# Optimization experiments

Hardware: AMD Instinct MI355X
Metric: run time of the kernel (lower is better)

Reference implementation:

```python
import jax, jax.numpy as jnp
import numpy as np

B, L, H, R, T = 2, 128, 768, 4, 3


def setup_inputs() -> dict:
    key = jax.random.key(0)
    ks = jax.random.split(key, 10)
    s = lambda k, shape: jax.random.normal(k, shape, dtype=jnp.float32) * 0.02
    return {
        "hidden_state": jax.random.normal(ks[0], (B, L, H), dtype=jnp.float32),
        "W_src": s(ks[1], (R * H, H)),
        "b_src": s(ks[2], (R * H,)),
        "W_tgt": s(ks[3], (R * H, H)),
        "b_tgt": s(ks[4], (R * H,)),
        "w_out": s(ks[5], (H,)),
        "dense_W": s(ks[6], (T * H, H)),
        "dense_b": s(ks[7], (T * H,)),
        "clf_W": s(ks[8], (1, H)),
        "clf_b": s(ks[9], (1,)),
    }


def reference(hidden_state, W_src, b_src, W_tgt, b_tgt, w_out,
              dense_W, dense_b, clf_W, clf_b):
    b, l, h = hidden_state.shape
    # Biaffine pairwise relation scoring (dropout = identity at eval).
    h_src = (hidden_state @ W_src.T + b_src).reshape(b, l, R, h)  # [B,L,R,H]
    h_tgt = (hidden_state @ W_tgt.T + b_tgt).reshape(b, l, R, h)  # [B,L,R,H]
    # Pairwise broadcast-add -> tanh -> reduce with w_out. [B,L,L,R,H] intermediate.
    pair = jnp.tanh(h_src[:, :, None, :, :] + h_tgt[:, None, :, :, :])
    relation_logits = jnp.einsum('bstrh,h->bstr', pair, w_out)
    relation_logits = jnp.transpose(relation_logits, (0, 3, 1, 2))  # [B,R,L,L]
    # Token binary classification head.
    z = (hidden_state @ dense_W.T + dense_b).reshape(b, l, T, h)   # [B,L,T,H]
    source_mask_logits = jnp.tanh(z) @ clf_W[0] + clf_b[0]          # [B,L,T]
    source_mask_logits = jnp.transpose(source_mask_logits, (0, 2, 1))  # [B,T,L]
    return relation_logits, source_mask_logits, h_src, h_tgt
```

## Files before the change

### kernel.cpp

```cpp
#include <hip/hip_runtime.h>
#include <hip/hip_bf16.h>

#define LL 128
#define HH 768
#define OFF_REL  0
#define OFF_MASK 131072
#define OFF_HSRC 131840
#define OFF_HTGT 918272
#define SCALEC 2.8853900817779268f

typedef __attribute__((ext_vector_type(8))) short short8;
typedef __attribute__((ext_vector_type(4))) float floatx4;

__device__ inline unsigned short f2bf(float f) {
  unsigned u = __float_as_uint(f);
  u += 0x7FFFu + ((u >> 16) & 1u);
  return (unsigned short)(u >> 16);
}
struct us4 { unsigned short x, y, z, w; };

__device__ __forceinline__ void gload16(const void* g, void* l) {
  __builtin_amdgcn_global_load_lds(
      (const __attribute__((address_space(1))) unsigned int*)g,
      (__attribute__((address_space(3))) unsigned int*)l,
      16, 0, 0);
}

__global__ __launch_bounds__(256) void cvt_kernel(
    const float4* __restrict__ hs, const float4* __restrict__ wsrc,
    const float4* __restrict__ wtgt, const float4* __restrict__ wd,
    us4* __restrict__ ab, us4* __restrict__ wb)
{
  const int n0 = 49152;
  const int n1 = n0 + 589824;
  const int n2 = n1 + 589824;
  const int n3 = n2 + 442368;
  int stride = gridDim.x * blockDim.x;
  for (int i = blockIdx.x * blockDim.x + threadIdx.x; i < n3; i += stride) {
    const float4* src; us4* dst;
    if (i < n0)      { src = hs   + i;        dst = ab + i; }
    else if (i < n1) { src = wsrc + (i - n0); dst = wb + (i - n0); }
    else if (i < n2) { src = wtgt + (i - n1); dst = wb + 589824 + (i - n1); }
    else             { src = wd   + (i - n2); dst = wb + 1179648 + (i - n2); }
    float4 v = *src;
    us4 o; o.x = f2bf(v.x); o.y = f2bf(v.y); o.z = f2bf(v.z); o.w = f2bf(v.w);
    *dst = o;
  }
}

__global__ __launch_bounds__(256, 2) void gemm_kernel(
    const unsigned short* __restrict__ Ab, const unsigned short* __restrict__ Wb,
    const float* __restrict__ b_src, const float* __restrict__ b_tgt,
    const float* __restrict__ dense_b,
    float* __restrict__ out, float* __restrict__ z,
    float* __restrict__ Es, float* __restrict__ Et)
{
  __shared__ __align__(1024) char sAB[4][16384];
  int tid = threadIdx.x;
  int wave = tid >> 6, lane = tid & 63;
  int nb = blockIdx.x, rb = blockIdx.y;
  int gcol0 = nb * 64, grow0 = rb * 64;
  int which = (nb < 48) ? 0 : (nb < 96) ? 1 : 2;

  int r0 = tid >> 3, c0 = tid & 7;
  int c0s = c0 ^ (r0 & 7);
  const unsigned short* gA0 = Ab + (long)(grow0 + r0) * HH + c0s * 8;
  const unsigned short* gA1 = gA0 + 32 * HH;
  const unsigned short* gB0 = Wb + (long)(gcol0 + r0) * HH + c0s * 8;
  const unsigned short* gB1 = gB0 + 32 * HH;

  int lr = lane & 15, hi = lane >> 4;
  int wm = (wave >> 1) * 32, wn = (wave & 1) * 32;
  int swz = lr & 7;

  floatx4 acc[2][2];
  #pragma unroll
  for (int mi = 0; mi < 2; ++mi)
    #pragma unroll
    for (int ni = 0; ni < 2; ++ni)
      acc[mi][ni] = (floatx4){0.f, 0.f, 0.f, 0.f};

#define STAGE(BUF, KT) do {                                       \
    char* b_ = &sAB[BUF][0];                                      \
    gload16(gA0 + (KT) * 64, b_ + wave * 1024);                   \
    gload16(gA1 + (KT) * 64, b_ + 4096 + wave * 1024);            \
    gload16(gB0 + (KT) * 64, b_ + 8192 + wave * 1024);            \
    gload16(gB1 + (KT) * 64, b_ + 12288 + wave * 1024);           \
  } while (0)

  STAGE(0, 0);
  STAGE(1, 1);
  STAGE(2, 2);

  #pragma unroll
  for (int kt = 0; kt < 12; ++kt) {
    int buf = kt & 3;
    if (kt <= 8) {
      STAGE((kt + 3) & 3, kt + 3);
      asm volatile("s_waitcnt vmcnt(12)" ::: "memory");
    } else if (kt == 9) {
      asm volatile("s_waitcnt vmcnt(8)" ::: "memory");
    } else if (kt == 10) {
      asm volatile("s_waitcnt vmcnt(4)" ::: "memory");
    } else {
      asm volatile("s_waitcnt vmcnt(0)" ::: "memory");
    }
    __builtin_amdgcn_sched_barrier(0);
    __builtin_amdgcn_s_barrier();
    __builtin_amdgcn_sched_barrier(0);

    const char* bA = &sAB[buf][0];
    const char* bB = bA + 8192;
    #pragma unroll
    for (int ks = 0; ks < 2; ++ks) {
      int cs = ((ks * 4 + hi) ^ swz) * 16;
      short8 a0 = *(const short8*)(bA + (wm + lr) * 128 + cs);
      short8 a1 = *(const short8*)(bA + (wm + 16 + lr) * 128 + cs);
      short8 b0 = *(const short8*)(bB + (wn + lr) * 128 + cs);
      short8 b1 = *(const short8*)(bB + (wn + 16 + lr) * 128 + cs);
      acc[0][0] = __builtin_amdgcn_mfma_f32_16x16x32_bf16(a0, b0, acc[0][0], 0, 0, 0);
      acc[0][1] = __builtin_amdgcn_mfma_f32_16x16x32_bf16(a0, b1, acc[0][1], 0, 0, 0);
      acc[1][0] = __builtin_amdgcn_mfma_f32_16x16x32_bf16(a1, b0, acc[1][0], 0, 0, 0);
      acc[1][1] = __builtin_amdgcn_mfma_f32_16x16x32_bf16(a1, b1, acc[1][1], 0, 0, 0);
    }

    __builtin_amdgcn_sched_barrier(0);
    __builtin_amdgcn_s_barrier();
  }
#undef STAGE

  int lrow = hi * 4;
  #pragma unroll
  for (int mi = 0; mi < 2; ++mi)
  #pragma unroll
  for (int ni = 0; ni < 2; ++ni) {
    int colg = gcol0 + wn + ni * 16 + lr;
    int row0 = grow0 + wm + mi * 16 + lrow;
    if (which == 0) {
      float bv = b_src[colg];
      #pragma unroll
      for (int r2 = 0; r2 < 4; ++r2) {
        int row = row0 + r2;
        float v = acc[mi][ni][r2] + bv;
        out[OFF_HSRC + row * 3072 + colg] = v;
        Es[row * 3072 + colg] = __builtin_amdgcn_exp2f(SCALEC * v);
      }
    } else if (which == 1) {
      int cc = colg - 3072;
      float bv = b_tgt[cc];
      #pragma unroll
      for (int r2 = 0; r2 < 4; ++r2) {
        int row = row0 + r2;
        float v = acc[mi][ni][r2] + bv;
        out[OFF_HTGT + row * 3072 + cc] = v;
        Et[row * 3072 + cc] = __builtin_amdgcn_exp2f(SCALEC * v);
      }
    } else {
      int cc = colg - 6144;
      float bv = dense_b[cc];
      #pragma unroll
      for (int r2 = 0; r2 < 4; ++r2)
        z[(row0 + r2) * 2304 + cc] = acc[mi][ni][r2] + bv;
    }
  }
}

#define PHC 256
__global__ __launch_bounds__(512) void pair_kernel(
    const float* __restrict__ Es, const float* __restrict__ Et,
    const float* __restrict__ w_out,
    const float* __restrict__ z, const float* __restrict__ clf_W,
    const float* __restrict__ clf_b, float* __restrict__ out)
{
  int tid = threadIdx.x;

  if (blockIdx.z == 8) {
    int blk = blockIdx.y * 8 + blockIdx.x;
    int wave = tid >> 6, lane = tid & 63;
    int slot = blk * 8 + wave;
    for (int o = slot; o < 768; o += 512) {
      int b = o / 384, rem = o - b * 384;
      int t = rem >> 7, lt = rem & 127;
      const float* zr = z + (long)(b * LL + lt) * 2304 + t * HH;
      float acc = 0.f;
      for (int h = lane; h < HH; h += 64) {
        float x = zr[h];
        float th = 1.f - 2.f * __builtin_amdgcn_rcpf(1.f + __builtin_amdgcn_exp2f(SCALEC * x));
        acc = fmaf(clf_W[h], th, acc);
      }
      #pragma unroll
      for (int d = 32; d; d >>= 1) acc += __shfl_down(acc, d);
      if (lane == 0) out[OFF_MASK + o] = acc + clf_b[0];
    }
    return;
  }

  __shared__ float sA[16][PHC + 4];
  __shared__ float sB[16][PHC + 4];
  __shared__ float sRed[2048];
  __shared__ float sWsum;

  int g = tid >> 6, lane = tid & 63;
  int sq = lane >> 3, tq = lane & 7;
  int t0 = blockIdx.x * 16, s0 = blockIdx.y * 16;
  int br = blockIdx.z, bb = br >> 2, r = br & 3;

  if (tid < 64) {
    float wsm = 0.f;
    for (int h = tid; h < HH; h += 64) wsm += w_out[h];
    #pragma unroll
    for (int d = 32; d; d >>= 1) wsm += __shfl_down(wsm, d);
    if (tid == 0) sWsum = wsm;
  }

  float a00 = 0.f, a01 = 0.f, a10 = 0.f, a11 = 0.f;

  for (int c = 0; c < HH; c += PHC) {
    int offu = __builtin_amdgcn_readfirstlane(c + g * 32);
    float4 wv[8];
    #pragma unroll
    for (int q = 0; q < 8; ++q) wv[q] = *(const float4*)(w_out + offu + q * 4);

    __syncthreads();
    #pragma unroll
    for (int j = 0; j < 2; ++j) {
      int idx = tid * 2 + j;
      int row = idx >> 6, col4 = (idx & 63) * 4;
      *(float4*)&sA[row][col4] =
          *(const float4*)(Es + (long)(bb * LL + s0 + row) * 3072 + r * HH + c + col4);
      *(float4*)&sB[row][col4] =
          *(const float4*)(Et + (long)(bb * LL + t0 + row) * 3072 + r * HH + c + col4);
    }
    __syncthreads();

    const float* pA0 = &sA[2 * sq][g * 32];
    const float* pA1 = &sA[2 * sq + 1][g * 32];
    const float* pB0 = &sB[2 * tq][g * 32];
    const float* pB1 = &sB[2 * tq + 1][g * 32];
    #pragma unroll
    for (int hh = 0; hh < 32; hh += 4) {
      float4 e0 = *(const float4*)(pA0 + hh);
      float4 e1 = *(const float4*)(pA1 + hh);
      float4 f0 = *(const float4*)(pB0 + hh);
      float4 f1 = *(const float4*)(pB1 + hh);
      float4 vw = wv[hh >> 2];
      a00 = fmaf(vw.x, __builtin_amdgcn_rcpf(fmaf(e0.x, f0.x, 1.f)), a00);
      a01 = fmaf(vw.x, __builtin_amdgcn_rcpf(fmaf(e0.x, f1.x, 1.f)), a01);
      a10 = fmaf(vw.x, __builtin_amdgcn_rcpf(fmaf(e1.x, f0.x, 1.f)), a10);
      a11 = fmaf(vw.x, __builtin_amdgcn_rcpf(fmaf(e1.x, f1.x, 1.f)), a11);
      a00 = fmaf(vw.y, __builtin_amdgcn_rcpf(fmaf(e0.y, f0.y, 1.f)), a00);
      a01 = fmaf(vw.y, __builtin_amdgcn_rcpf(fmaf(e0.y, f1.y, 1.f)), a01);
      a10 = fmaf(vw.y, __builtin_amdgcn_rcpf(fmaf(e1.y, f0.y, 1.f)), a10);
      a11 = fmaf(vw.y, __builtin_amdgcn_rcpf(fmaf(e1.y, f1.y, 1.f)), a11);
      a00 = fmaf(vw.z, __builtin_amdgcn_rcpf(fmaf(e0.z, f0.z, 1.f)), a00);
      a01 = fmaf(vw.z, __builtin_amdgcn_rcpf(fmaf(e0.z, f1.z, 1.f)), a01);
      a10 = fmaf(vw.z, __builtin_amdgcn_rcpf(fmaf(e1.z, f0.z, 1.f)), a10);
      a11 = fmaf(vw.z, __builtin_amdgcn_rcpf(fmaf(e1.z, f1.z, 1.f)), a11);
      a00 = fmaf(vw.w, __builtin_amdgcn_rcpf(fmaf(e0.w, f0.w, 1.f)), a00);
      a01 = fmaf(vw.w, __builtin_amdgcn_rcpf(fmaf(e0.w, f1.w, 1.f)), a01);
      a10 = fmaf(vw.w, __builtin_amdgcn_rcpf(fmaf(e1.w, f0.w, 1.f)), a10);
      a11 = fmaf(vw.w, __builtin_amdgcn_rcpf(fmaf(e1.w, f1.w, 1.f)), a11);
    }
  }

  sRed[0 * 512 + g * 64 + lane] = a00;
  sRed[1 * 512 + g * 64 + lane] = a01;
  sRed[2 * 512 + g * 64 + lane] = a10;
  sRed[3 * 512 + g * 64 + lane] = a11;
  __syncthreads();
  if (tid < 256) {
    int s = tid >> 4, t = tid & 15;
    int pp = (s >> 1) * 8 + (t >> 1);
    int sl = (s & 1) * 2 + (t & 1);
    float sum = 0.f;
    #pragma unroll
    for (int gg = 0; gg < 8; ++gg) sum += sRed[sl * 512 + gg * 64 + pp];
    out[((long)br * LL + (s0 + s)) * LL + (t0 + t)] = sWsum - 2.f * sum;
  }
}

extern "C" void kernel_launch(void* const* d_in, const int* in_sizes, int n_in,
                              void* d_out, int out_size, void* d_ws, size_t ws_size,
                              hipStream_t stream)
{
  const float* hidden  = (const float*)d_in[0];
  const float* W_src   = (const float*)d_in[1];
  const float* b_src   = (const float*)d_in[2];
  const float* W_tgt   = (const float*)d_in[3];
  const float* b_tgt   = (const float*)d_in[4];
  const float* w_out   = (const float*)d_in[5];
  const float* dense_W = (const float*)d_in[6];
  const float* dense_b = (const float*)d_in[7];
  const float* clf_W   = (const float*)d_in[8];
  const float* clf_b   = (const float*)d_in[9];
  float* out = (float*)d_out;
  char* ws = (char*)d_ws;

  unsigned short* Ab = (unsigned short*)ws;
  unsigned short* Wb = (unsigned short*)(ws + 393216);
  float* z  = (float*)(ws + 13369344);
  float* Es = (float*)(ws + 15728640);
  float* Et = (float*)(ws + 18874368);

  hipLaunchKernelGGL(cvt_kernel, dim3(2048), dim3(256), 0, stream,
      (const float4*)hidden, (const float4*)W_src, (const float4*)W_tgt,
      (const float4*)dense_W, (us4*)Ab, (us4*)Wb);
  hipLaunchKernelGGL(gemm_kernel, dim3(132, 4), dim3(256), 0, stream,
      Ab, Wb, b_src, b_tgt, dense_b, out, z, Es, Et);
  hipLaunchKernelGGL(pair_kernel, dim3(8, 8, 9), dim3(512), 0, stream,
      Es, Et, w_out, z, clf_W, clf_b, out + OFF_REL);
}
```

Measured before the change: 43.80 us.

## Store exp intermediates in bf16 and stage full hidden rows in LDS once

The GEMM epilogue now writes the exponentiated source and target projections as bf16 rather than fp32, halving that intermediate's write and read traffic. The pair kernel loads all 768 hidden columns for its 16x16 tile into shared memory in one pass, removing the three-chunk loop and its per-chunk barriers. w_out is also staged in LDS. The cost is lower precision in the exp values feeding the tanh reconstruction, a larger LDS footprint, and extra unpack work from bf16 to fp32 in the inner loop.

```diff
diff --git a/kernel.cpp b/kernel.cpp
--- a/kernel.cpp
+++ b/kernel.cpp
@@ -16,6 +16,9 @@
   unsigned u = __float_as_uint(f);
   u += 0x7FFFu + ((u >> 16) & 1u);
   return (unsigned short)(u >> 16);
+}
+__device__ __forceinline__ float bf2f(unsigned short u) {
+  return __uint_as_float(((unsigned)u) << 16);
 }
 struct us4 { unsigned short x, y, z, w; };
 
@@ -53,7 +56,7 @@
     const float* __restrict__ b_src, const float* __restrict__ b_tgt,
     const float* __restrict__ dense_b,
     float* __restrict__ out, float* __restrict__ z,
-    float* __restrict__ Es, float* __restrict__ Et)
+    unsigned short* __restrict__ Esb, unsigned short* __restrict__ Etb)
 {
   __shared__ __align__(1024) char sAB[4][16384];
   int tid = threadIdx.x;
@@ -143,7 +146,7 @@
         int row = row0 + r2;
         float v = acc[mi][ni][r2] + bv;
         out[OFF_HSRC + row * 3072 + colg] = v;
-        Es[row * 3072 + colg] = __builtin_amdgcn_exp2f(SCALEC * v);
+        Esb[row * 3072 + colg] = f2bf(__builtin_amdgcn_exp2f(SCALEC * v));
       }
     } else if (which == 1) {
       int cc = colg - 3072;
@@ -153,7 +156,7 @@
         int row = row0 + r2;
         float v = acc[mi][ni][r2] + bv;
         out[OFF_HTGT + row * 3072 + cc] = v;
-        Et[row * 3072 + cc] = __builtin_amdgcn_exp2f(SCALEC * v);
+        Etb[row * 3072 + cc] = f2bf(__builtin_amdgcn_exp2f(SCALEC * v));
       }
     } else {
       int cc = colg - 6144;
@@ -165,9 +168,9 @@
   }
 }
 
-#define PHC 256
+#define PADW 776
 __global__ __launch_bounds__(512) void pair_kernel(
-    const float* __restrict__ Es, const float* __restrict__ Et,
+    const unsigned short* __restrict__ Esb, const unsigned short* __restrict__ Etb,
     const float* __restrict__ w_out,
     const float* __restrict__ z, const float* __restrict__ clf_W,
     const float* __restrict__ clf_b, float* __restrict__ out)
@@ -195,8 +198,9 @@
     return;
   }
 
-  __shared__ float sA[16][PHC + 4];
-  __shared__ float sB[16][PHC + 4];
+  __shared__ unsigned short sA[16][PADW];
+  __shared__ unsigned short sB[16][PADW];
+  __shared__ __align__(16) float sW[768];
   __shared__ float sRed[2048];
   __shared__ float sWsum;
 
@@ -212,54 +216,46 @@
     for (int d = 32; d; d >>= 1) wsm += __shfl_down(wsm, d);
     if (tid == 0) sWsum = wsm;
   }
+  if (tid >= 64 && tid < 256) *(float4*)&sW[(tid - 64) * 4] = *(const float4*)(w_out + (tid - 64) * 4);
+
+  #pragma unroll
+  for (int j = 0; j < 3; ++j) {
+    int idx = j * 512 + tid;
+    int row = idx / 96, c8 = idx - row * 96;
+    *(uint4*)&sA[row][c8 * 8] =
+        *(const uint4*)(Esb + (long)(bb * LL + s0 + row) * 3072 + r * HH + c8 * 8);
+    *(uint4*)&sB[row][c8 * 8] =
+        *(const uint4*)(Etb + (long)(bb * LL + t0 + row) * 3072 + r * HH + c8 * 8);
+  }
+  __syncthreads();
 
   float a00 = 0.f, a01 = 0.f, a10 = 0.f, a11 = 0.f;
-
-  for (int c = 0; c < HH; c += PHC) {
-    int offu = __builtin_amdgcn_readfirstlane(c + g * 32);
-    float4 wv[8];
-    #pragma unroll
-    for (int q = 0; q < 8; ++q) wv[q] = *(const float4*)(w_out + offu + q * 4);
-
-    __syncthreads();
-    #pragma unroll
-    for (int j = 0; j < 2; ++j) {
-      int idx = tid * 2 + j;
-      int row = idx >> 6, col4 = (idx & 63) * 4;
-      *(float4*)&sA[row][col4] =
-          *(const float4*)(Es + (long)(bb * LL + s0 + row) * 3072 + r * HH + c + col4);
-      *(float4*)&sB[row][col4] =
-          *(const float4*)(Et + (long)(bb * LL + t0 + row) * 3072 + r * HH + c + col4);
-    }
-    __syncthreads();
-
-    const float* pA0 = &sA[2 * sq][g * 32];
-    const float* pA1 = &sA[2 * sq + 1][g * 32];
-    const float* pB0 = &sB[2 * tq][g * 32];
-    const float* pB1 = &sB[2 * tq + 1][g * 32];
-    #pragma unroll
-    for (int hh = 0; hh < 32; hh += 4) {
-      float4 e0 = *(const float4*)(pA0 + hh);
-      float4 e1 = *(const float4*)(pA1 + hh);
-      float4 f0 = *(const float4*)(pB0 + hh);
-      float4 f1 = *(const float4*)(pB1 + hh);
-      float4 vw = wv[hh >> 2];
-      a00 = fmaf(vw.x, __builtin_amdgcn_rcpf(fmaf(e0.x, f0.x, 1.f)), a00);
-      a01 = fmaf(vw.x, __builtin_amdgcn_rcpf(fmaf(e0.x, f1.x, 1.f)), a01);
-      a10 = fmaf(vw.x, __builtin_amdgcn_rcpf(fmaf(e1.x, f0.x, 1.f)), a10);
-      a11 = fmaf(vw.x, __builtin_amdgcn_rcpf(fmaf(e1.x, f1.x, 1.f)), a11);
-      a00 = fmaf(vw.y, __builtin_amdgcn_rcpf(fmaf(e0.y, f0.y, 1.f)), a00);
-      a01 = fmaf(vw.y, __builtin_amdgcn_rcpf(fmaf(e0.y, f1.y, 1.f)), a01);
-      a10 = fmaf(vw.y, __builtin_amdgcn_rcpf(fmaf(e1.y, f0.y, 1.f)), a10);
-      a11 = fmaf(vw.y, __builtin_amdgcn_rcpf(fmaf(e1.y, f1.y, 1.f)), a11);
-      a00 = fmaf(vw.z, __builtin_amdgcn_rcpf(fmaf(e0.z, f0.z, 1.f)), a00);
-      a01 = fmaf(vw.z, __builtin_amdgcn_rcpf(fmaf(e0.z, f1.z, 1.f)), a01);
-      a10 = fmaf(vw.z, __builtin_amdgcn_rcpf(fmaf(e1.z, f0.z, 1.f)), a10);
-      a11 = fmaf(vw.z, __builtin_amdgcn_rcpf(fmaf(e1.z, f1.z, 1.f)), a11);
-      a00 = fmaf(vw.w, __builtin_amdgcn_rcpf(fmaf(e0.w, f0.w, 1.f)), a00);
-      a01 = fmaf(vw.w, __builtin_amdgcn_rcpf(fmaf(e0.w, f1.w, 1.f)), a01);
-      a10 = fmaf(vw.w, __builtin_amdgcn_rcpf(fmaf(e1.w, f0.w, 1.f)), a10);
-      a11 = fmaf(vw.w, __builtin_amdgcn_rcpf(fmaf(e1.w, f1.w, 1.f)), a11);
+  const unsigned short* pA0 = &sA[2 * sq][g * 96];
+  const unsigned short* pA1 = &sA[2 * sq + 1][g * 96];
+  const unsigned short* pB0 = &sB[2 * tq][g * 96];
+  const unsigned short* pB1 = &sB[2 * tq + 1][g * 96];
+  const float* pW = &sW[g * 96];
+
+  #pragma unroll
+  for (int st = 0; st < 12; ++st) {
+    short8 ua0 = *(const short8*)(pA0 + st * 8);
+    short8 ua1 = *(const short8*)(pA1 + st * 8);
+    short8 ub0 = *(const short8*)(pB0 + st * 8);
+    short8 ub1 = *(const short8*)(pB1 + st * 8);
+    float4 wv0 = *(const float4*)(pW + st * 8);
+    float4 wv1 = *(const float4*)(pW + st * 8 + 4);
+    #pragma unroll
+    for (int q = 0; q < 8; ++q) {
+      float e0 = bf2f((unsigned short)ua0[q]);
+      float e1 = bf2f((unsigned short)ua1[q]);
+      float f0 = bf2f((unsigned short)ub0[q]);
+      float f1 = bf2f((unsigned short)ub1[q]);
+      float w = (q < 4) ? ((q == 0) ? wv0.x : (q == 1) ? wv0.y : (q == 2) ? wv0.z : wv0.w)
+                        : ((q == 4) ? wv1.x : (q == 5) ? wv1.y : (q == 6) ? wv1.z : wv1.w);
+      a00 = fmaf(w, __builtin_amdgcn_rcpf(fmaf(e0, f0, 1.f)), a00);
+      a01 = fmaf(w, __builtin_amdgcn_rcpf(fmaf(e0, f1, 1.f)), a01);
+      a10 = fmaf(w, __builtin_amdgcn_rcpf(fmaf(e1, f0, 1.f)), a10);
+      a11 = fmaf(w, __builtin_amdgcn_rcpf(fmaf(e1, f1, 1.f)), a11);
     }
   }
 
@@ -296,17 +292,17 @@
   float* out = (float*)d_out;
   char* ws = (char*)d_ws;
 
-  unsigned short* Ab = (unsigned short*)ws;
-  unsigned short* Wb = (unsigned short*)(ws + 393216);
-  float* z  = (float*)(ws + 13369344);
-  float* Es = (float*)(ws + 15728640);
-  float* Et = (float*)(ws + 18874368);
+  unsigned short* Ab  = (unsigned short*)ws;
+  unsigned short* Wb  = (unsigned short*)(ws + 393216);
+  float* z            = (float*)(ws + 13369344);
+  unsigned short* Esb = (unsigned short*)(ws + 15728640);
+  unsigned short* Etb = (unsigned short*)(ws + 17301504);
 
   hipLaunchKernelGGL(cvt_kernel, dim3(2048), dim3(256), 0, stream,
       (const float4*)hidden, (const float4*)W_src, (const float4*)W_tgt,
       (const float4*)dense_W, (us4*)Ab, (us4*)Wb);
   hipLaunchKernelGGL(gemm_kernel, dim3(132, 4), dim3(256), 0, stream,
-      Ab, Wb, b_src, b_tgt, dense_b, out, z, Es, Et);
+      Ab, Wb, b_src, b_tgt, dense_b, out, z, Esb, Etb);
   hipLaunchKernelGGL(pair_kernel, dim3(8, 8, 9), dim3(512), 0, stream,
-      Es, Et, w_out, z, clf_W, clf_b, out + OFF_REL);
-}
+      Esb, Etb, w_out, z, clf_W, clf_b, out + OFF_REL);
+}
```

New measurement: 47.93 us. +9.4%, slower.
